# Kernel optimization log

Measured on AMD Instinct MI355X. Metric: run time of the kernel, lower is better.

The kernel has to match this reference:

```python
import jax, jax.numpy as jnp
import numpy as np
from jax.ops import segment_sum

N_NODES = 100000
N_EDGES = 1600000
N_GRAPHS = 64
IN_DIM = 128
HID = 128
N_CLASSES = 10


def setup_inputs() -> dict:
    key = jax.random.key(0)
    ks = jax.random.split(key, 8)
    h = jax.random.normal(ks[0], (N_NODES, IN_DIM), dtype=jnp.float32)
    src = jax.random.randint(ks[1], (N_EDGES,), 0, N_NODES, dtype=jnp.int64)
    dst = jax.random.randint(ks[2], (N_EDGES,), 0, N_NODES, dtype=jnp.int64)
    graph_ids = jnp.sort(jax.random.randint(ks[3], (N_NODES,), 0, N_GRAPHS, dtype=jnp.int64))
    # Glorot-ish scaled weights
    W1 = jax.random.normal(ks[4], (IN_DIM, HID), dtype=jnp.float32) / np.sqrt(IN_DIM)
    b1 = jnp.zeros((HID,), dtype=jnp.float32)
    W2 = jax.random.normal(ks[5], (HID, HID), dtype=jnp.float32) / np.sqrt(HID)
    b2 = jnp.zeros((HID,), dtype=jnp.float32)
    Wc = jax.random.normal(ks[6], (HID, N_CLASSES), dtype=jnp.float32) / np.sqrt(HID)
    bc = jnp.zeros((N_CLASSES,), dtype=jnp.float32)
    return {"h": h, "src": src, "dst": dst, "graph_ids": graph_ids,
            "W1": W1, "b1": b1, "W2": W2, "b2": b2, "Wc": Wc, "bc": bc}


def _graph_conv(h, src, dst, W, b, n_nodes):
    # DGL GraphConv, norm='both': D_out^{-1/2} scaling of src feats,
    # sum aggregation over edges, D_in^{-1/2} scaling of dst, then XW + b.
    ones = jnp.ones((src.shape[0],), dtype=h.dtype)
    deg_out = jnp.clip(segment_sum(ones, src, num_segments=n_nodes), 1.0)
    deg_in = jnp.clip(segment_sum(ones, dst, num_segments=n_nodes), 1.0)
    hn = h * jax.lax.rsqrt(deg_out)[:, None]          # [N, d]
    agg = segment_sum(hn[src], dst, num_segments=n_nodes)  # SpMM: [N, d]
    agg = agg * jax.lax.rsqrt(deg_in)[:, None]
    return agg @ W + b


def reference(h, src, dst, graph_ids, W1, b1, W2, b2, Wc, bc):
    n = h.shape[0]
    x = jax.nn.relu(_graph_conv(h, src, dst, W1, b1, n))
    x = jax.nn.relu(_graph_conv(x, src, dst, W2, b2, n))
    # mean_nodes readout per graph
    counts = jnp.clip(segment_sum(jnp.ones((n,), x.dtype), graph_ids, num_segments=N_GRAPHS), 1.0)
    hg = segment_sum(x, graph_ids, num_segments=N_GRAPHS) / counts[:, None]  # [G, d]
    return hg @ Wc + bc  # [G, n_classes]
```

## Files before the change

kernel.cpp:

```cpp
#include <hip/hip_runtime.h>

#define DIM 128
#define NG 64
#define NCLS 10
#define CAP 64
#define WSZ 256
#define NWMAX 512
#define CAPB 8192
#define EPB 8192
#define HL 4
#define WTP 68

typedef __attribute__((ext_vector_type(8))) short s8v;
typedef __attribute__((ext_vector_type(4))) float f4v;

__device__ inline unsigned short f2bf(float f) {
    unsigned int u = __float_as_uint(f);
    unsigned int r = (u + 0x7fffu + ((u >> 16) & 1u)) >> 16;
    return (unsigned short)r;
}
__device__ inline unsigned int pack2bf(float a, float b) {
    return ((unsigned int)f2bf(b) << 16) | (unsigned int)f2bf(a);
}

__global__ void prep_kernel(const float* __restrict__ W1, const float* __restrict__ W2,
                            unsigned short* __restrict__ Wt1, unsigned short* __restrict__ Wt2,
                            int* curD, int* curS, uint4* hb4, uint4* x1b4,
                            float* __restrict__ hg, int nw, int n) {
    int t = blockIdx.x * 256 + threadIdx.x;
    if (t < nw) {
        curD[t] = t * CAPB;
        curS[t] = t * CAPB;
    }
    if (t < 32768) {
        int which = t >> 14;
        int i = t & 16383;
        int c = i >> 7, k = i & 127;
        (which ? Wt2 : Wt1)[i] = f2bf((which ? W2 : W1)[k * 128 + c]);
    }
    if (t < NG * DIM) hg[t] = 0.0f;
    if (t < 16) {
        uint4 z = make_uint4(0, 0, 0, 0);
        hb4[(size_t)n * 16 + t] = z;
        x1b4[(size_t)n * 16 + t] = z;
    }
}

__global__ __launch_bounds__(1024) void bucket_kernel(const int* __restrict__ src,
                                                      const int* __restrict__ dst,
                                                      int* curD, int* curS,
                                                      int* __restrict__ bucketD,
                                                      unsigned char* __restrict__ bucketS,
                                                      int e, int nw) {
    __shared__ int histD[NWMAX];
    __shared__ int histS[NWMAX];
    int t = threadIdx.x;
    for (int i = t; i < nw; i += 1024) { histD[i] = 0; histS[i] = 0; }
    __syncthreads();
    int lo = blockIdx.x * EPB;
    int hi = min(e, lo + EPB);
    for (int i = lo + t * 4; i < hi; i += 4096) {
        int4 d4 = *(const int4*)&dst[i];
        int4 s4 = *(const int4*)&src[i];
        atomicAdd(&histD[d4.x >> 8], 1); atomicAdd(&histS[s4.x >> 8], 1);
        atomicAdd(&histD[d4.y >> 8], 1); atomicAdd(&histS[s4.y >> 8], 1);
        atomicAdd(&histD[d4.z >> 8], 1); atomicAdd(&histS[s4.z >> 8], 1);
        atomicAdd(&histD[d4.w >> 8], 1); atomicAdd(&histS[s4.w >> 8], 1);
    }
    __syncthreads();
    for (int i = t; i < nw; i += 1024) {
        int hd = histD[i], hs = histS[i];
        histD[i] = hd ? atomicAdd(&curD[i], hd) : 0;
        histS[i] = hs ? atomicAdd(&curS[i], hs) : 0;
    }
    __syncthreads();
    for (int i = lo + t * 4; i < hi; i += 4096) {
        int4 d4 = *(const int4*)&dst[i];
        int4 s4 = *(const int4*)&src[i];
#pragma unroll
        for (int j = 0; j < 4; ++j) {
            int d = (&d4.x)[j], s = (&s4.x)[j];
            int sd = atomicAdd(&histD[d >> 8], 1);
            bucketD[sd] = (s << 8) | (d & 255);
            int ss = atomicAdd(&histS[s >> 8], 1);
            bucketS[ss] = (unsigned char)(s & 255);
        }
    }
}

__global__ __launch_bounds__(512) void window_kernel(const int* __restrict__ curD,
                                                     const int* __restrict__ curS,
                                                     const int* __restrict__ bucketD,
                                                     const unsigned char* __restrict__ bucketS,
                                                     const float* __restrict__ h,
                                                     int* __restrict__ cnt_in,
                                                     float* __restrict__ rs_in,
                                                     float* __restrict__ rs_out,
                                                     int* __restrict__ colx_pad,
                                                     uint4* __restrict__ hb4, int n) {
    __shared__ int cin[WSZ];
    __shared__ int cout[WSZ];
    __shared__ float rsO_s[WSZ];
    int w = blockIdx.x, t = threadIdx.x;
    if (t < WSZ) { cin[t] = 0; cout[t] = 0; }
    __syncthreads();
    int base = w * CAPB;
    int nE = min(curD[w] - base, CAPB);
    for (int i = t; i < nE; i += 512) {
        int v = bucketD[base + i];
        int d8 = v & 255;
        int slot = atomicAdd(&cin[d8], 1);
        if (slot < CAP) colx_pad[(((w << 8) + d8) << 6) + slot] = v >> 8;
    }
    int nS = min(curS[w] - base, CAPB);
    for (int i = t; i < nS; i += 512) atomicAdd(&cout[bucketS[base + i]], 1);
    __syncthreads();
    if (t < WSZ) {
        int node = (w << 8) + t;
        if (node < n) {
            int c = cin[t];
            cnt_in[node] = c;
            rs_in[node] = rsqrtf(fmaxf((float)c, 1.0f));
            float ro = rsqrtf(fmaxf((float)cout[t], 1.0f));
            rs_out[node] = ro;
            rsO_s[t] = ro;
            int cc = min(c, CAP);
            int c8 = min((cc + 7) & ~7, CAP);
            for (int s = cc; s < c8; ++s) colx_pad[((size_t)node << 6) + s] = n;
        }
    }
    __syncthreads();
    for (int idx = t; idx < WSZ * 16; idx += 512) {
        int rl = idx >> 4, sub = idx & 15;
        int nd = (w << 8) + rl;
        if (nd < n) {
            float s = rsO_s[rl];
            float4 a = ((const float4*)h)[(size_t)nd * 32 + sub * 2];
            float4 b = ((const float4*)h)[(size_t)nd * 32 + sub * 2 + 1];
            uint4 o;
            o.x = pack2bf(a.x * s, a.y * s);
            o.y = pack2bf(a.z * s, a.w * s);
            o.z = pack2bf(b.x * s, b.y * s);
            o.w = pack2bf(b.z * s, b.w * s);
            hb4[(size_t)nd * 16 + sub] = o;
        }
    }
}

__global__ __launch_bounds__(256) void spmm_bf16(const uint4* __restrict__ xb4,
                                                 const int* __restrict__ cnt_in,
                                                 const int* __restrict__ colx_pad,
                                                 const float* __restrict__ rs_in,
                                                 uint4* __restrict__ yb4, int n) {
    int node = (blockIdx.x * 256 + threadIdx.x) >> 6;
    int lane = threadIdx.x & 63;
    if (node >= n) return;
    int g = lane >> 4, sub = lane & 15;
    int cnt = min(cnt_in[node], CAP);
    int cnt8 = min((cnt + 7) & ~7, CAP);
    int myc = colx_pad[((size_t)node << 6) + ((lane < cnt8) ? lane : 0)];
    float acc[8] = {0.f, 0.f, 0.f, 0.f, 0.f, 0.f, 0.f, 0.f};
    int j = 0;
    for (; j + 16 <= cnt8; j += 16) {
        uint4 v[4];
#pragma unroll
        for (int b = 0; b < 4; ++b) {
            int c = __shfl(myc, j + 4 * b + g);
            v[b] = xb4[(size_t)c * 16 + sub];
        }
#pragma unroll
        for (int b = 0; b < 4; ++b) {
            acc[0] += __uint_as_float(v[b].x << 16);
            acc[1] += __uint_as_float(v[b].x & 0xffff0000u);
            acc[2] += __uint_as_float(v[b].y << 16);
            acc[3] += __uint_as_float(v[b].y & 0xffff0000u);
            acc[4] += __uint_as_float(v[b].z << 16);
            acc[5] += __uint_as_float(v[b].z & 0xffff0000u);
            acc[6] += __uint_as_float(v[b].w << 16);
            acc[7] += __uint_as_float(v[b].w & 0xffff0000u);
        }
    }
    if (j < cnt8) {
        int c0 = __shfl(myc, j + g);
        int c1 = __shfl(myc, j + 4 + g);
        uint4 v0 = xb4[(size_t)c0 * 16 + sub];
        uint4 v1 = xb4[(size_t)c1 * 16 + sub];
#pragma unroll
        for (int b = 0; b < 2; ++b) {
            uint4 v = b ? v1 : v0;
            acc[0] += __uint_as_float(v.x << 16);
            acc[1] += __uint_as_float(v.x & 0xffff0000u);
            acc[2] += __uint_as_float(v.y << 16);
            acc[3] += __uint_as_float(v.y & 0xffff0000u);
            acc[4] += __uint_as_float(v.z << 16);
            acc[5] += __uint_as_float(v.z & 0xffff0000u);
            acc[6] += __uint_as_float(v.w << 16);
            acc[7] += __uint_as_float(v.w & 0xffff0000u);
        }
    }
#pragma unroll
    for (int i = 0; i < 8; ++i) {
        acc[i] += __shfl_xor(acc[i], 16);
        acc[i] += __shfl_xor(acc[i], 32);
    }
    if (g == 0) {
        float w = rs_in[node];
        uint4 o;
        o.x = pack2bf(acc[0] * w, acc[1] * w);
        o.y = pack2bf(acc[2] * w, acc[3] * w);
        o.z = pack2bf(acc[4] * w, acc[5] * w);
        o.w = pack2bf(acc[6] * w, acc[7] * w);
        yb4[(size_t)node * 16 + sub] = o;
    }
}

__device__ inline void stage_wt(const uint4* __restrict__ Wt4, unsigned int* WtL, int t) {
#pragma unroll
    for (int i = 0; i < 8; ++i) {
        int q = t + 256 * i;
        int row = q >> 4, col4 = q & 15;
        *(uint4*)&WtL[row * WTP + col4 * 4] = Wt4[q];
    }
}

__global__ __launch_bounds__(256) void mm_mfma(const unsigned char* __restrict__ A,
                                               const uint4* __restrict__ Wt4,
                                               const float* __restrict__ bias,
                                               const float* __restrict__ rs_out,
                                               unsigned short* __restrict__ out, int n) {
    __shared__ unsigned int WtL[128 * WTP];
    int t = threadIdx.x;
    stage_wt(Wt4, WtL, t);
    int wave = t >> 6, lane = t & 63;
    int m = lane & 15, q = lane >> 4;
    int r0 = (int)blockIdx.x * 64 + wave * 16;
    int arow = min(r0 + m, n - 1);
    __syncthreads();
    f4v acc[8];
#pragma unroll
    for (int c = 0; c < 8; ++c) acc[c] = (f4v){0.f, 0.f, 0.f, 0.f};
#pragma unroll
    for (int k0 = 0; k0 < 4; ++k0) {
        s8v a = *(const s8v*)(A + (size_t)arow * 256 + k0 * 64 + q * 16);
#pragma unroll
        for (int c = 0; c < 8; ++c) {
            s8v b = *(const s8v*)&WtL[(c * 16 + m) * WTP + k0 * 16 + q * 4];
            acc[c] = __builtin_amdgcn_mfma_f32_16x16x32_bf16(a, b, acc[c], 0, 0, 0);
        }
    }
#pragma unroll
    for (int c = 0; c < 8; ++c) {
        float bv = bias[c * 16 + m];
#pragma unroll
        for (int r = 0; r < 4; ++r) {
            int row = r0 + q * 4 + r;
            if (row < n) {
                float val = fmaxf(acc[c][r] + bv, 0.0f);
                out[(size_t)row * 128 + c * 16 + m] = f2bf(val * rs_out[row]);
            }
        }
    }
}

__global__ __launch_bounds__(256) void mm_mfma_readout(const unsigned char* __restrict__ A,
                                                       const uint4* __restrict__ Wt4,
                                                       const float* __restrict__ bias,
                                                       const int* __restrict__ gid,
                                                       float* __restrict__ hg, int n) {
    __shared__ unsigned int WtL[128 * WTP];
    __shared__ float hgloc[HL][DIM];
    int t = threadIdx.x;
    stage_wt(Wt4, WtL, t);
    for (int i = t; i < HL * DIM; i += 256) ((float*)hgloc)[i] = 0.0f;
    int wave = t >> 6, lane = t & 63;
    int m = lane & 15, q = lane >> 4;
    int r0 = (int)blockIdx.x * 64 + wave * 16;
    int b0 = (int)blockIdx.x * 64;
    int gid0 = gid[min(b0, n - 1)];
    int arow = min(r0 + m, n - 1);
    __syncthreads();
    f4v acc[8];
#pragma unroll
    for (int c = 0; c < 8; ++c) acc[c] = (f4v){0.f, 0.f, 0.f, 0.f};
#pragma unroll
    for (int k0 = 0; k0 < 4; ++k0) {
        s8v a = *(const s8v*)(A + (size_t)arow * 256 + k0 * 64 + q * 16);
#pragma unroll
        for (int c = 0; c < 8; ++c) {
            s8v b = *(const s8v*)&WtL[(c * 16 + m) * WTP + k0 * 16 + q * 4];
            acc[c] = __builtin_amdgcn_mfma_f32_16x16x32_bf16(a, b, acc[c], 0, 0, 0);
        }
    }
    int gfirst = gid[min(r0, n - 1)];
    int glast = gid[min(r0 + 15, n - 1)];
    bool uni = (gfirst == glast) && (r0 + 15 < n);
    if (uni) {
        int gl = gfirst - gid0;
#pragma unroll
        for (int c = 0; c < 8; ++c) {
            float bv = bias[c * 16 + m];
            float s = fmaxf(acc[c][0] + bv, 0.0f) + fmaxf(acc[c][1] + bv, 0.0f) +
                      fmaxf(acc[c][2] + bv, 0.0f) + fmaxf(acc[c][3] + bv, 0.0f);
            s += __shfl_xor(s, 16);
            s += __shfl_xor(s, 32);
            if (q == 0) {
                if (gl < HL)
                    atomicAdd(&hgloc[gl][c * 16 + m], s);
                else
                    atomicAdd(&hg[(size_t)gfirst * DIM + c * 16 + m], s);
            }
        }
    } else {
#pragma unroll
        for (int r = 0; r < 4; ++r) {
            int row = r0 + q * 4 + r;
            if (row < n) {
                int g = gid[row];
                int gl = g - gid0;
#pragma unroll
                for (int c = 0; c < 8; ++c) {
                    float val = fmaxf(acc[c][r] + bias[c * 16 + m], 0.0f);
                    if (gl < HL)
                        atomicAdd(&hgloc[gl][c * 16 + m], val);
                    else
                        atomicAdd(&hg[(size_t)g * DIM + c * 16 + m], val);
                }
            }
        }
    }
    __syncthreads();
    for (int i = t; i < HL * DIM; i += 256) {
        float v = ((float*)hgloc)[i];
        int g = gid0 + (i >> 7);
        if (v != 0.0f && g < NG) atomicAdd(&hg[(size_t)g * DIM + (i & 127)], v);
    }
}

__global__ void classify_kernel(const float* __restrict__ hg, const int* __restrict__ gid,
                                const float* __restrict__ Wc, const float* __restrict__ bc,
                                float* __restrict__ out, int n) {
    __shared__ float inv;
    int g = blockIdx.x, t = threadIdx.x;
    if (t == 0) {
        int lo = 0, hi = n;
        while (lo < hi) { int mid = (lo + hi) >> 1; if (gid[mid] < g) lo = mid + 1; else hi = mid; }
        int lb = lo;
        lo = 0; hi = n;
        while (lo < hi) { int mid = (lo + hi) >> 1; if (gid[mid] <= g) lo = mid + 1; else hi = mid; }
        inv = 1.0f / fmaxf((float)(lo - lb), 1.0f);
    }
    __syncthreads();
    if (t < NCLS) {
        float s = 0.0f;
        for (int k = 0; k < DIM; ++k) s = fmaf(hg[g * DIM + k], Wc[k * NCLS + t], s);
        out[g * NCLS + t] = s * inv + bc[t];
    }
}

extern "C" void kernel_launch(void* const* d_in, const int* in_sizes, int n_in,
                              void* d_out, int out_size, void* d_ws, size_t ws_size,
                              hipStream_t stream) {
    const float* h   = (const float*)d_in[0];
    const int*   src = (const int*)d_in[1];
    const int*   dst = (const int*)d_in[2];
    const int*   gid = (const int*)d_in[3];
    const float* W1  = (const float*)d_in[4];
    const float* b1  = (const float*)d_in[5];
    const float* W2  = (const float*)d_in[6];
    const float* b2  = (const float*)d_in[7];
    const float* Wc  = (const float*)d_in[8];
    const float* bc  = (const float*)d_in[9];
    float* out = (float*)d_out;

    const int n = in_sizes[0] / DIM;
    const int e = in_sizes[1];
    const int nw = (n + WSZ - 1) / WSZ;

    char* ws = (char*)d_ws;
    size_t off = 0;
    auto alloc = [&](size_t bytes) -> char* {
        char* p = ws + off;
        off = (off + bytes + 255) & ~(size_t)255;
        return p;
    };
    int*   cnt_in  = (int*)alloc((size_t)n * 4);
    float* rs_in   = (float*)alloc((size_t)n * 4);
    float* rs_out  = (float*)alloc((size_t)n * 4);
    int*   curD    = (int*)alloc((size_t)NWMAX * 4);
    int*   curS    = (int*)alloc((size_t)NWMAX * 4);
    int*   colx_pad = (int*)alloc((size_t)n * CAP * 4);
    int*   bucketD = (int*)alloc((size_t)nw * CAPB * 4);
    unsigned char* bucketS = (unsigned char*)alloc((size_t)nw * CAPB);
    float* hg      = (float*)alloc((size_t)NG * DIM * 4);
    unsigned short* Wt1 = (unsigned short*)alloc(128 * 128 * 2);
    unsigned short* Wt2 = (unsigned short*)alloc(128 * 128 * 2);
    uint4* hb4  = (uint4*)alloc((size_t)(n + 4) * 64 * 4);
    uint4* aggB = (uint4*)alloc((size_t)(n + 4) * 64 * 4);
    uint4* x1b4 = (uint4*)alloc((size_t)(n + 4) * 64 * 4);

    const int SPMM_B = (n + 3) / 4;
    const int MM_B = (n + 63) / 64;
    const int AB = (e + EPB - 1) / EPB;

    prep_kernel<<<128, 256, 0, stream>>>(W1, W2, Wt1, Wt2, curD, curS, hb4, x1b4, hg, nw, n);
    bucket_kernel<<<AB, 1024, 0, stream>>>(src, dst, curD, curS, bucketD, bucketS, e, nw);
    window_kernel<<<nw, 512, 0, stream>>>(curD, curS, bucketD, bucketS, h,
                                          cnt_in, rs_in, rs_out, colx_pad, hb4, n);

    spmm_bf16<<<SPMM_B, 256, 0, stream>>>(hb4, cnt_in, colx_pad, rs_in, aggB, n);
    mm_mfma<<<MM_B, 256, 0, stream>>>((const unsigned char*)aggB, (const uint4*)Wt1,
                                      b1, rs_out, (unsigned short*)x1b4, n);
    spmm_bf16<<<SPMM_B, 256, 0, stream>>>(x1b4, cnt_in, colx_pad, rs_in, aggB, n);
    mm_mfma_readout<<<MM_B, 256, 0, stream>>>((const unsigned char*)aggB, (const uint4*)Wt2,
                                              b2, gid, hg, n);
    classify_kernel<<<NG, 64, 0, stream>>>(hg, gid, Wc, bc, out, n);
}
```

Baseline: 309.4 us.

## Fold prep into bucket kernel, memset cursors, widen window and MFMA blocks

```diff
diff --git a/kernel.cpp b/kernel.cpp
--- a/kernel.cpp
+++ b/kernel.cpp
@@ -7,7 +7,7 @@
 #define WSZ 256
 #define NWMAX 512
 #define CAPB 8192
-#define EPB 8192
+#define EPB 4096
 #define HL 4
 #define WTP 68
 
@@ -21,29 +21,6 @@
 }
 __device__ inline unsigned int pack2bf(float a, float b) {
     return ((unsigned int)f2bf(b) << 16) | (unsigned int)f2bf(a);
-}
-
-__global__ void prep_kernel(const float* __restrict__ W1, const float* __restrict__ W2,
-                            unsigned short* __restrict__ Wt1, unsigned short* __restrict__ Wt2,
-                            int* curD, int* curS, uint4* hb4, uint4* x1b4,
-                            float* __restrict__ hg, int nw, int n) {
-    int t = blockIdx.x * 256 + threadIdx.x;
-    if (t < nw) {
-        curD[t] = t * CAPB;
-        curS[t] = t * CAPB;
-    }
-    if (t < 32768) {
-        int which = t >> 14;
-        int i = t & 16383;
-        int c = i >> 7, k = i & 127;
-        (which ? Wt2 : Wt1)[i] = f2bf((which ? W2 : W1)[k * 128 + c]);
-    }
-    if (t < NG * DIM) hg[t] = 0.0f;
-    if (t < 16) {
-        uint4 z = make_uint4(0, 0, 0, 0);
-        hb4[(size_t)n * 16 + t] = z;
-        x1b4[(size_t)n * 16 + t] = z;
-    }
 }
 
 __global__ __launch_bounds__(1024) void bucket_kernel(const int* __restrict__ src,
@@ -51,10 +28,29 @@
                                                       int* curD, int* curS,
                                                       int* __restrict__ bucketD,
                                                       unsigned char* __restrict__ bucketS,
-                                                      int e, int nw) {
+                                                      const float* __restrict__ W1,
+                                                      const float* __restrict__ W2,
+                                                      unsigned short* __restrict__ Wt1,
+                                                      unsigned short* __restrict__ Wt2,
+                                                      float* __restrict__ hg,
+                                                      uint4* hb4, uint4* x1b4,
+                                                      int e, int nw, int n) {
     __shared__ int histD[NWMAX];
     __shared__ int histS[NWMAX];
     int t = threadIdx.x;
+    int gtid = blockIdx.x * 1024 + t;
+    if (gtid < 32768) {
+        int which = gtid >> 14;
+        int i = gtid & 16383;
+        int c = i >> 7, k = i & 127;
+        (which ? Wt2 : Wt1)[i] = f2bf((which ? W2 : W1)[k * 128 + c]);
+    }
+    if (gtid < NG * DIM) hg[gtid] = 0.0f;
+    if (gtid < 16) {
+        uint4 z = make_uint4(0, 0, 0, 0);
+        hb4[(size_t)n * 16 + gtid] = z;
+        x1b4[(size_t)n * 16 + gtid] = z;
+    }
     for (int i = t; i < nw; i += 1024) { histD[i] = 0; histS[i] = 0; }
     __syncthreads();
     int lo = blockIdx.x * EPB;
@@ -81,39 +77,39 @@
         for (int j = 0; j < 4; ++j) {
             int d = (&d4.x)[j], s = (&s4.x)[j];
             int sd = atomicAdd(&histD[d >> 8], 1);
-            bucketD[sd] = (s << 8) | (d & 255);
+            bucketD[(size_t)(d >> 8) * CAPB + sd] = (s << 8) | (d & 255);
             int ss = atomicAdd(&histS[s >> 8], 1);
-            bucketS[ss] = (unsigned char)(s & 255);
-        }
-    }
-}
-
-__global__ __launch_bounds__(512) void window_kernel(const int* __restrict__ curD,
-                                                     const int* __restrict__ curS,
-                                                     const int* __restrict__ bucketD,
-                                                     const unsigned char* __restrict__ bucketS,
-                                                     const float* __restrict__ h,
-                                                     int* __restrict__ cnt_in,
-                                                     float* __restrict__ rs_in,
-                                                     float* __restrict__ rs_out,
-                                                     int* __restrict__ colx_pad,
-                                                     uint4* __restrict__ hb4, int n) {
+            bucketS[(size_t)(s >> 8) * CAPB + ss] = (unsigned char)(s & 255);
+        }
+    }
+}
+
+__global__ __launch_bounds__(1024) void window_kernel(const int* __restrict__ curD,
+                                                      const int* __restrict__ curS,
+                                                      const int* __restrict__ bucketD,
+                                                      const unsigned char* __restrict__ bucketS,
+                                                      const float* __restrict__ h,
+                                                      int* __restrict__ cnt_in,
+                                                      float* __restrict__ rs_in,
+                                                      float* __restrict__ rs_out,
+                                                      int* __restrict__ colx_pad,
+                                                      uint4* __restrict__ hb4, int n) {
     __shared__ int cin[WSZ];
     __shared__ int cout[WSZ];
     __shared__ float rsO_s[WSZ];
     int w = blockIdx.x, t = threadIdx.x;
     if (t < WSZ) { cin[t] = 0; cout[t] = 0; }
     __syncthreads();
-    int base = w * CAPB;
-    int nE = min(curD[w] - base, CAPB);
-    for (int i = t; i < nE; i += 512) {
+    size_t base = (size_t)w * CAPB;
+    int nE = min(curD[w], CAPB);
+    for (int i = t; i < nE; i += 1024) {
         int v = bucketD[base + i];
         int d8 = v & 255;
         int slot = atomicAdd(&cin[d8], 1);
         if (slot < CAP) colx_pad[(((w << 8) + d8) << 6) + slot] = v >> 8;
     }
-    int nS = min(curS[w] - base, CAPB);
-    for (int i = t; i < nS; i += 512) atomicAdd(&cout[bucketS[base + i]], 1);
+    int nS = min(curS[w], CAPB);
+    for (int i = t; i < nS; i += 1024) atomicAdd(&cout[bucketS[base + i]], 1);
     __syncthreads();
     if (t < WSZ) {
         int node = (w << 8) + t;
@@ -130,7 +126,7 @@
         }
     }
     __syncthreads();
-    for (int idx = t; idx < WSZ * 16; idx += 512) {
+    for (int idx = t; idx < WSZ * 16; idx += 1024) {
         int rl = idx >> 4, sub = idx & 15;
         int nd = (w << 8) + rl;
         if (nd < n) {
@@ -233,30 +229,34 @@
     stage_wt(Wt4, WtL, t);
     int wave = t >> 6, lane = t & 63;
     int m = lane & 15, q = lane >> 4;
-    int r0 = (int)blockIdx.x * 64 + wave * 16;
-    int arow = min(r0 + m, n - 1);
-    __syncthreads();
-    f4v acc[8];
-#pragma unroll
-    for (int c = 0; c < 8; ++c) acc[c] = (f4v){0.f, 0.f, 0.f, 0.f};
-#pragma unroll
-    for (int k0 = 0; k0 < 4; ++k0) {
-        s8v a = *(const s8v*)(A + (size_t)arow * 256 + k0 * 64 + q * 16);
+    __syncthreads();
+#pragma unroll
+    for (int rg = 0; rg < 2; ++rg) {
+        int r0 = (int)blockIdx.x * 128 + rg * 64 + wave * 16;
+        if (r0 >= n) break;
+        int arow = min(r0 + m, n - 1);
+        f4v acc[8];
+#pragma unroll
+        for (int c = 0; c < 8; ++c) acc[c] = (f4v){0.f, 0.f, 0.f, 0.f};
+#pragma unroll
+        for (int k0 = 0; k0 < 4; ++k0) {
+            s8v a = *(const s8v*)(A + (size_t)arow * 256 + k0 * 64 + q * 16);
+#pragma unroll
+            for (int c = 0; c < 8; ++c) {
+                s8v b = *(const s8v*)&WtL[(c * 16 + m) * WTP + k0 * 16 + q * 4];
+                acc[c] = __builtin_amdgcn_mfma_f32_16x16x32_bf16(a, b, acc[c], 0, 0, 0);
+            }
+        }
 #pragma unroll
         for (int c = 0; c < 8; ++c) {
-            s8v b = *(const s8v*)&WtL[(c * 16 + m) * WTP + k0 * 16 + q * 4];
-            acc[c] = __builtin_amdgcn_mfma_f32_16x16x32_bf16(a, b, acc[c], 0, 0, 0);
-        }
-    }
-#pragma unroll
-    for (int c = 0; c < 8; ++c) {
-        float bv = bias[c * 16 + m];
-#pragma unroll
-        for (int r = 0; r < 4; ++r) {
-            int row = r0 + q * 4 + r;
-            if (row < n) {
-                float val = fmaxf(acc[c][r] + bv, 0.0f);
-                out[(size_t)row * 128 + c * 16 + m] = f2bf(val * rs_out[row]);
+            float bv = bias[c * 16 + m];
+#pragma unroll
+            for (int r = 0; r < 4; ++r) {
+                int row = r0 + q * 4 + r;
+                if (row < n) {
+                    float val = fmaxf(acc[c][r] + bv, 0.0f);
+                    out[(size_t)row * 128 + c * 16 + m] = f2bf(val * rs_out[row]);
+                }
             }
         }
     }
@@ -274,56 +274,60 @@
     for (int i = t; i < HL * DIM; i += 256) ((float*)hgloc)[i] = 0.0f;
     int wave = t >> 6, lane = t & 63;
     int m = lane & 15, q = lane >> 4;
-    int r0 = (int)blockIdx.x * 64 + wave * 16;
-    int b0 = (int)blockIdx.x * 64;
+    int b0 = (int)blockIdx.x * 128;
     int gid0 = gid[min(b0, n - 1)];
-    int arow = min(r0 + m, n - 1);
-    __syncthreads();
-    f4v acc[8];
-#pragma unroll
-    for (int c = 0; c < 8; ++c) acc[c] = (f4v){0.f, 0.f, 0.f, 0.f};
-#pragma unroll
-    for (int k0 = 0; k0 < 4; ++k0) {
-        s8v a = *(const s8v*)(A + (size_t)arow * 256 + k0 * 64 + q * 16);
-#pragma unroll
-        for (int c = 0; c < 8; ++c) {
-            s8v b = *(const s8v*)&WtL[(c * 16 + m) * WTP + k0 * 16 + q * 4];
-            acc[c] = __builtin_amdgcn_mfma_f32_16x16x32_bf16(a, b, acc[c], 0, 0, 0);
-        }
-    }
-    int gfirst = gid[min(r0, n - 1)];
-    int glast = gid[min(r0 + 15, n - 1)];
-    bool uni = (gfirst == glast) && (r0 + 15 < n);
-    if (uni) {
-        int gl = gfirst - gid0;
-#pragma unroll
-        for (int c = 0; c < 8; ++c) {
-            float bv = bias[c * 16 + m];
-            float s = fmaxf(acc[c][0] + bv, 0.0f) + fmaxf(acc[c][1] + bv, 0.0f) +
-                      fmaxf(acc[c][2] + bv, 0.0f) + fmaxf(acc[c][3] + bv, 0.0f);
-            s += __shfl_xor(s, 16);
-            s += __shfl_xor(s, 32);
-            if (q == 0) {
-                if (gl < HL)
-                    atomicAdd(&hgloc[gl][c * 16 + m], s);
-                else
-                    atomicAdd(&hg[(size_t)gfirst * DIM + c * 16 + m], s);
+    __syncthreads();
+#pragma unroll
+    for (int rg = 0; rg < 2; ++rg) {
+        int r0 = b0 + rg * 64 + wave * 16;
+        if (r0 >= n) break;
+        int arow = min(r0 + m, n - 1);
+        f4v acc[8];
+#pragma unroll
+        for (int c = 0; c < 8; ++c) acc[c] = (f4v){0.f, 0.f, 0.f, 0.f};
+#pragma unroll
+        for (int k0 = 0; k0 < 4; ++k0) {
+            s8v a = *(const s8v*)(A + (size_t)arow * 256 + k0 * 64 + q * 16);
+#pragma unroll
+            for (int c = 0; c < 8; ++c) {
+                s8v b = *(const s8v*)&WtL[(c * 16 + m) * WTP + k0 * 16 + q * 4];
+                acc[c] = __builtin_amdgcn_mfma_f32_16x16x32_bf16(a, b, acc[c], 0, 0, 0);
             }
         }
-    } else {
-#pragma unroll
-        for (int r = 0; r < 4; ++r) {
-            int row = r0 + q * 4 + r;
-            if (row < n) {
-                int g = gid[row];
-                int gl = g - gid0;
-#pragma unroll
-                for (int c = 0; c < 8; ++c) {
-                    float val = fmaxf(acc[c][r] + bias[c * 16 + m], 0.0f);
+        int gfirst = gid[min(r0, n - 1)];
+        int glast = gid[min(r0 + 15, n - 1)];
+        bool uni = (gfirst == glast) && (r0 + 15 < n);
+        if (uni) {
+            int gl = gfirst - gid0;
+#pragma unroll
+            for (int c = 0; c < 8; ++c) {
+                float bv = bias[c * 16 + m];
+                float s = fmaxf(acc[c][0] + bv, 0.0f) + fmaxf(acc[c][1] + bv, 0.0f) +
+                          fmaxf(acc[c][2] + bv, 0.0f) + fmaxf(acc[c][3] + bv, 0.0f);
+                s += __shfl_xor(s, 16);
+                s += __shfl_xor(s, 32);
+                if (q == 0) {
                     if (gl < HL)
-                        atomicAdd(&hgloc[gl][c * 16 + m], val);
+                        atomicAdd(&hgloc[gl][c * 16 + m], s);
                     else
-                        atomicAdd(&hg[(size_t)g * DIM + c * 16 + m], val);
+                        atomicAdd(&hg[(size_t)gfirst * DIM + c * 16 + m], s);
+                }
+            }
+        } else {
+#pragma unroll
+            for (int r = 0; r < 4; ++r) {
+                int row = r0 + q * 4 + r;
+                if (row < n) {
+                    int g = gid[row];
+                    int gl = g - gid0;
+#pragma unroll
+                    for (int c = 0; c < 8; ++c) {
+                        float val = fmaxf(acc[c][r] + bias[c * 16 + m], 0.0f);
+                        if (gl < HL)
+                            atomicAdd(&hgloc[gl][c * 16 + m], val);
+                        else
+                            atomicAdd(&hg[(size_t)g * DIM + c * 16 + m], val);
+                    }
                 }
             }
         }
@@ -386,8 +390,8 @@
     int*   cnt_in  = (int*)alloc((size_t)n * 4);
     float* rs_in   = (float*)alloc((size_t)n * 4);
     float* rs_out  = (float*)alloc((size_t)n * 4);
-    int*   curD    = (int*)alloc((size_t)NWMAX * 4);
-    int*   curS    = (int*)alloc((size_t)NWMAX * 4);
+    int*   curD    = (int*)alloc((size_t)2 * NWMAX * 4);
+    int*   curS    = curD + NWMAX;
     int*   colx_pad = (int*)alloc((size_t)n * CAP * 4);
     int*   bucketD = (int*)alloc((size_t)nw * CAPB * 4);
     unsigned char* bucketS = (unsigned char*)alloc((size_t)nw * CAPB);
@@ -399,13 +403,15 @@
     uint4* x1b4 = (uint4*)alloc((size_t)(n + 4) * 64 * 4);
 
     const int SPMM_B = (n + 3) / 4;
-    const int MM_B = (n + 63) / 64;
+    const int MM_B = (n + 127) / 128;
     const int AB = (e + EPB - 1) / EPB;
 
-    prep_kernel<<<128, 256, 0, stream>>>(W1, W2, Wt1, Wt2, curD, curS, hb4, x1b4, hg, nw, n);
-    bucket_kernel<<<AB, 1024, 0, stream>>>(src, dst, curD, curS, bucketD, bucketS, e, nw);
-    window_kernel<<<nw, 512, 0, stream>>>(curD, curS, bucketD, bucketS, h,
-                                          cnt_in, rs_in, rs_out, colx_pad, hb4, n);
+    (void)hipMemsetAsync(curD, 0, (size_t)2 * NWMAX * 4, stream);
+
+    bucket_kernel<<<AB, 1024, 0, stream>>>(src, dst, curD, curS, bucketD, bucketS,
+                                           W1, W2, Wt1, Wt2, hg, hb4, x1b4, e, nw, n);
+    window_kernel<<<nw, 1024, 0, stream>>>(curD, curS, bucketD, bucketS, h,
+                                           cnt_in, rs_in, rs_out, colx_pad, hb4, n);
 
     spmm_bf16<<<SPMM_B, 256, 0, stream>>>(hb4, cnt_in, colx_pad, rs_in, aggB, n);
     mm_mfma<<<MM_B, 256, 0, stream>>>((const unsigned char*)aggB, (const uint4*)Wt1,
```

Result: slower. 320.0 us (+3.4%).
